# Kernel optimization log

Measured on AMD Instinct MI355X. Metric: run time of the kernel, lower is better.

Reference implementation:

```python
import jax, jax.numpy as jnp
import numpy as np

BETA = 0.5        # membrane decay (from source)
THRESHOLD = 1.0   # snn.Leaky default
ALPHA = 2.0       # ATan surrogate default slope (snntorch)


@jax.custom_vjp
def spike_fn(v):
    # Heaviside spike: 1 where membrane - threshold > 0
    return (v > 0).astype(v.dtype)


def _spike_fwd(v):
    return spike_fn(v), v


def _spike_bwd(v, g):
    # snntorch ATan surrogate gradient: (alpha/2) / (1 + (pi/2*alpha*v)^2)
    grad = (ALPHA / 2.0) / (1.0 + (jnp.pi / 2.0 * ALPHA * v) ** 2)
    return (g * grad,)


spike_fn.defvjp(_spike_fwd, _spike_bwd)


def setup_inputs() -> dict:
    key = jax.random.key(0)
    # x: [T, B, N] = [num_steps, batch, neurons]
    x = jax.random.normal(key, (128, 64, 4096), dtype=jnp.float32)
    return {"x": x}


def reference(x):
    # snntorch Leaky with init_hidden=True, reset_mechanism='subtract':
    #   reset_t = H(mem_{t-1} - thr)
    #   mem_t   = beta*mem_{t-1} + x_t - reset_t*thr
    #   spk_t   = H(mem_t - thr)
    mem0 = jnp.zeros(x.shape[1:], dtype=x.dtype)

    def step(mem, xt):
        reset = spike_fn(mem - THRESHOLD)
        mem_new = BETA * mem + xt - reset * THRESHOLD
        spk = spike_fn(mem_new - THRESHOLD)
        return mem_new, spk

    _, spk_rec = jax.lax.scan(step, mem0, x)  # spk_rec: [T, B, N]
    return spk_rec
```

## Files before the change

kernel.cpp:

```cpp
#include <hip/hip_runtime.h>


#define T_STEPS 128
#define UNROLL 8

__global__ __launch_bounds__(256) void snn_leaky_fwd(const float4* __restrict__ x,
                                                     float4* __restrict__ out,
                                                     int n4) {
    const int idx = blockIdx.x * blockDim.x + threadIdx.x;
    if (idx >= n4) return;

    const float4* xp = x + idx;
    float4* op = out + idx;

    float4 mem = make_float4(0.f, 0.f, 0.f, 0.f);

    for (int t = 0; t < T_STEPS; t += UNROLL) {
        float4 xt[UNROLL];
#pragma unroll
        for (int u = 0; u < UNROLL; ++u) {
            xt[u] = xp[(size_t)(t + u) * (size_t)n4];
        }
#pragma unroll
        for (int u = 0; u < UNROLL; ++u) {
            const float4 v = xt[u];
            float4 spk;
            mem.x = 0.5f * mem.x + v.x - (mem.x > 1.0f ? 1.0f : 0.0f);
            mem.y = 0.5f * mem.y + v.y - (mem.y > 1.0f ? 1.0f : 0.0f);
            mem.z = 0.5f * mem.z + v.z - (mem.z > 1.0f ? 1.0f : 0.0f);
            mem.w = 0.5f * mem.w + v.w - (mem.w > 1.0f ? 1.0f : 0.0f);
            spk.x = mem.x > 1.0f ? 1.0f : 0.0f;
            spk.y = mem.y > 1.0f ? 1.0f : 0.0f;
            spk.z = mem.z > 1.0f ? 1.0f : 0.0f;
            spk.w = mem.w > 1.0f ? 1.0f : 0.0f;
            op[(size_t)(t + u) * (size_t)n4] = spk;
        }
    }
}

extern "C" void kernel_launch(void* const* d_in, const int* in_sizes, int n_in,
                              void* d_out, int out_size, void* d_ws, size_t ws_size,
                              hipStream_t stream) {
    const float4* x = (const float4*)d_in[0];
    float4* out = (float4*)d_out;

    const int total = in_sizes[0];
    const int nstep = total / T_STEPS;
    const int n4 = nstep / 4;

    const int block = 256;
    const int grid = (n4 + block - 1) / block;
    snn_leaky_fwd<<<grid, block, 0, stream>>>(x, out, n4);
}
```

Baseline: 227.2 us.

## Use scalar per-thread neurons with software-pipelined loads and nontemporal stores

Each thread now handles one neuron instead of four, launching four times as many threads for more parallelism. The time loop is software-pipelined: the next 16 timesteps are loaded while the current 16 are computed. Outputs use nontemporal stores to avoid polluting the cache. The trade-off is narrower 4-byte memory accesses instead of 16-byte vector accesses, plus higher register pressure from the 32-element buffers.

```diff
diff --git a/kernel.cpp b/kernel.cpp
--- a/kernel.cpp
+++ b/kernel.cpp
@@ -2,53 +2,54 @@
 
 
 #define T_STEPS 128
-#define UNROLL 8
+#define U 16
 
-__global__ __launch_bounds__(256) void snn_leaky_fwd(const float4* __restrict__ x,
-                                                     float4* __restrict__ out,
-                                                     int n4) {
+__global__ __launch_bounds__(256) void snn_leaky_fwd(const float* __restrict__ x,
+                                                     float* __restrict__ out,
+                                                     int n) {
     const int idx = blockIdx.x * blockDim.x + threadIdx.x;
-    if (idx >= n4) return;
+    if (idx >= n) return;
 
-    const float4* xp = x + idx;
-    float4* op = out + idx;
+    const float* xp = x + idx;
+    float* op = out + idx;
 
-    float4 mem = make_float4(0.f, 0.f, 0.f, 0.f);
+    float mem = 0.0f;
+    float cur[U], nxt[U];
 
-    for (int t = 0; t < T_STEPS; t += UNROLL) {
-        float4 xt[UNROLL];
 #pragma unroll
-        for (int u = 0; u < UNROLL; ++u) {
-            xt[u] = xp[(size_t)(t + u) * (size_t)n4];
+    for (int u = 0; u < U; ++u) cur[u] = xp[(size_t)u * n];
+
+    for (int t = 0; t < T_STEPS - U; t += U) {
+#pragma unroll
+        for (int u = 0; u < U; ++u) nxt[u] = xp[(size_t)(t + U + u) * n];
+#pragma unroll
+        for (int u = 0; u < U; ++u) {
+            mem = 0.5f * mem + cur[u] - (mem > 1.0f ? 1.0f : 0.0f);
+            float spk = (mem > 1.0f) ? 1.0f : 0.0f;
+            __builtin_nontemporal_store(spk, op + (size_t)(t + u) * n);
         }
 #pragma unroll
-        for (int u = 0; u < UNROLL; ++u) {
-            const float4 v = xt[u];
-            float4 spk;
-            mem.x = 0.5f * mem.x + v.x - (mem.x > 1.0f ? 1.0f : 0.0f);
-            mem.y = 0.5f * mem.y + v.y - (mem.y > 1.0f ? 1.0f : 0.0f);
-            mem.z = 0.5f * mem.z + v.z - (mem.z > 1.0f ? 1.0f : 0.0f);
-            mem.w = 0.5f * mem.w + v.w - (mem.w > 1.0f ? 1.0f : 0.0f);
-            spk.x = mem.x > 1.0f ? 1.0f : 0.0f;
-            spk.y = mem.y > 1.0f ? 1.0f : 0.0f;
-            spk.z = mem.z > 1.0f ? 1.0f : 0.0f;
-            spk.w = mem.w > 1.0f ? 1.0f : 0.0f;
-            op[(size_t)(t + u) * (size_t)n4] = spk;
-        }
+        for (int u = 0; u < U; ++u) cur[u] = nxt[u];
+    }
+
+#pragma unroll
+    for (int u = 0; u < U; ++u) {
+        mem = 0.5f * mem + cur[u] - (mem > 1.0f ? 1.0f : 0.0f);
+        float spk = (mem > 1.0f) ? 1.0f : 0.0f;
+        __builtin_nontemporal_store(spk, op + (size_t)(T_STEPS - U + u) * n);
     }
 }
 
 extern "C" void kernel_launch(void* const* d_in, const int* in_sizes, int n_in,
                               void* d_out, int out_size, void* d_ws, size_t ws_size,
                               hipStream_t stream) {
-    const float4* x = (const float4*)d_in[0];
-    float4* out = (float4*)d_out;
+    const float* x = (const float*)d_in[0];
+    float* out = (float*)d_out;
 
     const int total = in_sizes[0];
-    const int nstep = total / T_STEPS;
-    const int n4 = nstep / 4;
+    const int n = total / T_STEPS;
 
     const int block = 256;
-    const int grid = (n4 + block - 1) / block;
-    snn_leaky_fwd<<<grid, block, 0, stream>>>(x, out, n4);
+    const int grid = (n + block - 1) / block;
+    snn_leaky_fwd<<<grid, block, 0, stream>>>(x, out, n);
 }
```

Result: slower. 234.0 us (+3.0%).

## Split time scan across two blocks with redundant warm-up and rolling prefetch

Applied to the files above, without the earlier changes.

The grid is doubled to 512 blocks. Phase-0 blocks compute and store the first 64 time steps. Phase-1 blocks rerun the first 64 steps without storing, to rebuild the membrane state, and then store steps 64-127. Loads now go through an 8-deep rolling register buffer instead of batched groups of 8. This is meant to expose more parallelism to hide memory latency in the sequential scan, at the cost of reading half the input twice. The indexing hardcodes 256 chunks and drops the bounds check, so it assumes this exact shape.

```diff
diff --git a/kernel.cpp b/kernel.cpp
--- a/kernel.cpp
+++ b/kernel.cpp
@@ -2,38 +2,59 @@
 
 
 #define T_STEPS 128
-#define UNROLL 8
+#define T_HALF 64
+#define D 8
+
+__device__ __forceinline__ float4 lif_step(float4& mem, const float4 v) {
+    mem.x = 0.5f * mem.x + v.x - (mem.x > 1.0f ? 1.0f : 0.0f);
+    mem.y = 0.5f * mem.y + v.y - (mem.y > 1.0f ? 1.0f : 0.0f);
+    mem.z = 0.5f * mem.z + v.z - (mem.z > 1.0f ? 1.0f : 0.0f);
+    mem.w = 0.5f * mem.w + v.w - (mem.w > 1.0f ? 1.0f : 0.0f);
+    float4 s;
+    s.x = mem.x > 1.0f ? 1.0f : 0.0f;
+    s.y = mem.y > 1.0f ? 1.0f : 0.0f;
+    s.z = mem.z > 1.0f ? 1.0f : 0.0f;
+    s.w = mem.w > 1.0f ? 1.0f : 0.0f;
+    return s;
+}
 
 __global__ __launch_bounds__(256) void snn_leaky_fwd(const float4* __restrict__ x,
                                                      float4* __restrict__ out,
                                                      int n4) {
-    const int idx = blockIdx.x * blockDim.x + threadIdx.x;
-    if (idx >= n4) return;
+    const int chunk = blockIdx.x & 255;
+    const int phase = blockIdx.x >> 8;
+    const int col = chunk * 256 + threadIdx.x;
 
-    const float4* xp = x + idx;
-    float4* op = out + idx;
+    const float4* xp = x + col;
+    float4* op = out + col;
 
+    float4 buf[D];
     float4 mem = make_float4(0.f, 0.f, 0.f, 0.f);
 
-    for (int t = 0; t < T_STEPS; t += UNROLL) {
-        float4 xt[UNROLL];
 #pragma unroll
-        for (int u = 0; u < UNROLL; ++u) {
-            xt[u] = xp[(size_t)(t + u) * (size_t)n4];
+    for (int u = 0; u < D; ++u) buf[u] = xp[(size_t)u * n4];
+
+    if (phase == 0) {
+#pragma unroll
+        for (int t = 0; t < T_HALF; ++t) {
+            const float4 v = buf[t % D];
+            if (t + D < T_HALF) buf[t % D] = xp[(size_t)(t + D) * n4];
+            const float4 s = lif_step(mem, v);
+            op[(size_t)t * n4] = s;
+        }
+    } else {
+#pragma unroll
+        for (int t = 0; t < T_HALF; ++t) {
+            const float4 v = buf[t % D];
+            buf[t % D] = xp[(size_t)(t + D) * n4];
+            (void)lif_step(mem, v);
         }
 #pragma unroll
-        for (int u = 0; u < UNROLL; ++u) {
-            const float4 v = xt[u];
-            float4 spk;
-            mem.x = 0.5f * mem.x + v.x - (mem.x > 1.0f ? 1.0f : 0.0f);
-            mem.y = 0.5f * mem.y + v.y - (mem.y > 1.0f ? 1.0f : 0.0f);
-            mem.z = 0.5f * mem.z + v.z - (mem.z > 1.0f ? 1.0f : 0.0f);
-            mem.w = 0.5f * mem.w + v.w - (mem.w > 1.0f ? 1.0f : 0.0f);
-            spk.x = mem.x > 1.0f ? 1.0f : 0.0f;
-            spk.y = mem.y > 1.0f ? 1.0f : 0.0f;
-            spk.z = mem.z > 1.0f ? 1.0f : 0.0f;
-            spk.w = mem.w > 1.0f ? 1.0f : 0.0f;
-            op[(size_t)(t + u) * (size_t)n4] = spk;
+        for (int t = T_HALF; t < T_STEPS; ++t) {
+            const float4 v = buf[t % D];
+            if (t + D < T_STEPS) buf[t % D] = xp[(size_t)(t + D) * n4];
+            const float4 s = lif_step(mem, v);
+            op[(size_t)t * n4] = s;
         }
     }
 }
@@ -45,10 +66,7 @@
     float4* out = (float4*)d_out;
 
     const int total = in_sizes[0];
-    const int nstep = total / T_STEPS;
-    const int n4 = nstep / 4;
+    const int n4 = total / T_STEPS / 4;
 
-    const int block = 256;
-    const int grid = (n4 + block - 1) / block;
-    snn_leaky_fwd<<<grid, block, 0, stream>>>(x, out, n4);
+    snn_leaky_fwd<<<512, 256, 0, stream>>>(x, out, n4);
 }
```

Result: no change. 226.2 us (-0.5%).
